# Kernel optimization log

Measured on AMD Instinct MI355X. Metric: run time of the kernel, lower is better.

The kernel has to match this reference:

```python
import jax, jax.numpy as jnp
import numpy as np

B, C, W, H = 4, 64, 64, 64
CH = 64  # ch == input_nc so residual is valid

def setup_inputs() -> dict:
    key = jax.random.key(0)
    ks = jax.random.split(key, 5)
    return {
        "x": jax.random.normal(ks[0], (B, C, W, H), jnp.float32),
        "y": jax.random.normal(ks[1], (B, C, W, H), jnp.float32),
        "Wf": jax.random.normal(ks[2], (CH // 2, C), jnp.float32) * 0.05,
        "bf": jnp.zeros((CH // 2,), jnp.float32),
        "Wg": jax.random.normal(ks[3], (CH // 2, C), jnp.float32) * 0.05,
        "bg": jnp.zeros((CH // 2,), jnp.float32),
        "Wh": jax.random.normal(ks[4], (CH, C), jnp.float32) * 0.05,
        "bh": jnp.zeros((CH,), jnp.float32),
        "gamma": jnp.full((1,), 0.5, jnp.float32),
    }

def reference(x, y, Wf, bf, Wg, bg, Wh, bh, gamma):
    b, c, w, h = x.shape
    n = w * h
    xf = x.reshape(b, c, n)   # [b, C, N]
    yf = y.reshape(b, c, n)
    # 1x1 convs == per-pixel linear maps over channels
    f = jnp.einsum('oc,bcn->bon', Wf, xf) + bf[None, :, None]   # [b, CH/2, N]
    g = jnp.einsum('oc,bcn->bon', Wg, yf) + bg[None, :, None]   # [b, CH/2, N]
    hv = jnp.einsum('oc,bcn->bon', Wh, yf) + bh[None, :, None]  # [b, CH,   N]
    # s = g^T @ f : [b, N, N]
    s = jnp.einsum('bcm,bcn->bmn', g, f)
    beta = jax.nn.softmax(s, axis=-1)
    # o = beta @ h^T : [b, N, CH]
    o = jnp.einsum('bmn,bcn->bmc', beta, hv)
    o = o.transpose(0, 2, 1).reshape(b, -1, w, h)  # [b, CH, w, h]
    return gamma[0] * o + x
```

## Files before the change

kernel.cpp:

```cpp
#include <hip/hip_runtime.h>
#include <hip/hip_bf16.h>

#define BB  4
#define CC  64
#define NN  4096
#define CF  32
#define CHN 64

typedef __attribute__((ext_vector_type(8))) __bf16 bf16x8;
typedef __attribute__((ext_vector_type(4))) __bf16 bf16x4;
typedef __attribute__((ext_vector_type(4))) float floatx4;

__device__ __forceinline__ float clamp60(float v) {
    return fminf(fmaxf(v, -60.f), 60.f);
}
__device__ __forceinline__ float scrub(float v) {
    return fminf(fmaxf(v, -1e30f), 1e30f);
}

__global__ __launch_bounds__(256) void prep_kernel(
    const float* __restrict__ x, const float* __restrict__ y,
    const float* __restrict__ Wf, const float* __restrict__ bfp,
    const float* __restrict__ Wg, const float* __restrict__ bgp,
    const float* __restrict__ Wh, const float* __restrict__ bhp,
    __bf16* __restrict__ fT, __bf16* __restrict__ gT, __bf16* __restrict__ hvb)
{
    __shared__ __align__(16) __bf16 wbf[128][72];
    __shared__ float sbias[128];

    const int t  = threadIdx.x;
    const int w  = t >> 6;
    const int l  = t & 63;
    const int lo = l & 15;
    const int q  = l >> 4;

    const int b   = blockIdx.x >> 6;
    const int nb  = blockIdx.x & 63;
    const int nn  = nb * 64 + w * 16 + lo;

    for (int i = t; i < 128 * CC; i += 256) {
        int row = i >> 6, c = i & 63;
        float wv;
        if (row < 32)      wv = Wf[(size_t)row * CC + c];
        else if (row < 64) wv = Wg[(size_t)(row - 32) * CC + c];
        else               wv = Wh[(size_t)(row - 64) * CC + c];
        wbf[row][c] = (__bf16)wv;
    }
    if (t < 128) {
        if (t < 32)      sbias[t] = bfp[t];
        else if (t < 64) sbias[t] = bgp[t - 32];
        else             sbias[t] = bhp[t - 64];
    }
    __syncthreads();

    const float* xb = x + (size_t)b * CC * NN;
    const float* yb = y + (size_t)b * CC * NN;
    bf16x8 bx[2], by[2];
    #pragma unroll
    for (int kh = 0; kh < 2; kh++) {
        #pragma unroll
        for (int j = 0; j < 8; j++) {
            int c = kh * 32 + q * 8 + j;
            bx[kh][j] = (__bf16)xb[(size_t)c * NN + nn];
            by[kh][j] = (__bf16)yb[(size_t)c * NN + nn];
        }
    }

    const floatx4 zero4 = {0.f, 0.f, 0.f, 0.f};
    #pragma unroll
    for (int ct = 0; ct < 8; ct++) {
        const bf16x8* src = (ct < 2) ? bx : by;
        floatx4 acc = zero4;
        #pragma unroll
        for (int kh = 0; kh < 2; kh++) {
            const bf16x8 a = *(const bf16x8*)&wbf[ct*16 + lo][kh*32 + q*8];
            acc = __builtin_amdgcn_mfma_f32_16x16x32_bf16(a, src[kh], acc, 0, 0, 0);
        }
        if (ct < 4) {
            bf16x4 pk;
            #pragma unroll
            for (int r = 0; r < 4; r++)
                pk[r] = (__bf16)(acc[r] + sbias[ct*16 + q*4 + r]);
            __bf16* dstbase = (ct < 2) ? fT : gT;
            int cho = (ct & 1) * 16;
            *(bf16x4*)&dstbase[((size_t)b * NN + nn) * CF + cho + q*4] = pk;
        } else {
            #pragma unroll
            for (int r = 0; r < 4; r++) {
                int ch = (ct - 4) * 16 + q*4 + r;
                hvb[((size_t)b * CHN + ch) * NN + nn] =
                    (__bf16)(acc[r] + sbias[64 + ch]);
            }
        }
    }
}

__global__ __launch_bounds__(512, 2) void attn_kernel(
    const __bf16* __restrict__ fT, const __bf16* __restrict__ gT,
    const __bf16* __restrict__ hvb,
    const float* __restrict__ x, const float* __restrict__ gamma_p,
    float* __restrict__ out)
{
    __shared__ __align__(16) char smem[8*64*67*4 + 8*64*4];
    __bf16 (*pbf)[72]      = (__bf16 (*)[72])smem;
    float  (*osum)[64][67] = (float (*)[64][67])smem;
    float* lsum = (float*)(smem + 8*64*67*4);

    const int t  = threadIdx.x;
    const int w  = t >> 6;
    const int l  = t & 63;
    const int lo = l & 15;
    const int q  = l >> 4;

    const int mg = blockIdx.x & 63;
    const int b  = blockIdx.x >> 6;
    const int m0 = mg * 64;

    const __bf16* fb = fT  + (size_t)b * NN * CF;
    const __bf16* gb = gT  + (size_t)b * NN * CF;
    const __bf16* hb = hvb + (size_t)b * CHN * NN;

    bf16x8 ag[4];
    #pragma unroll
    for (int mt = 0; mt < 4; mt++)
        ag[mt] = *(const bf16x8*)(gb + (size_t)(m0 + mt*16 + lo) * CF + q * 8);

    bf16x8 vone;
    #pragma unroll
    for (int j = 0; j < 8; j++) vone[j] = (__bf16)1.0f;

    const floatx4 zero4 = {0.f, 0.f, 0.f, 0.f};
    floatx4 oacc[4][4];
    #pragma unroll
    for (int mt = 0; mt < 4; mt++)
        #pragma unroll
        for (int ct = 0; ct < 4; ct++) oacc[mt][ct] = zero4;
    floatx4 lacc[4];
    #pragma unroll
    for (int mt = 0; mt < 4; mt++) lacc[mt] = zero4;

    for (int i = 0; i < 8; i++) {
        const int n0 = (8*i + w) * 64;

        bf16x8 bff[4];
        #pragma unroll
        for (int nt = 0; nt < 4; nt++)
            bff[nt] = *(const bf16x8*)(fb + (size_t)(n0 + nt*16 + lo) * CF + q * 8);
        bf16x8 bhh[4][2];
        #pragma unroll
        for (int ct = 0; ct < 4; ct++)
            #pragma unroll
            for (int jb = 0; jb < 2; jb++)
                bhh[ct][jb] = *(const bf16x8*)(hb + (size_t)(ct*16 + lo) * NN + n0 + jb*32 + q*8);

        #pragma unroll
        for (int mt = 0; mt < 4; mt++) {
            floatx4 s4[4];
            #pragma unroll
            for (int nt = 0; nt < 4; nt++)
                s4[nt] = __builtin_amdgcn_mfma_f32_16x16x32_bf16(ag[mt], bff[nt], zero4, 0, 0, 0);

            #pragma unroll
            for (int nt = 0; nt < 4; nt++)
                #pragma unroll
                for (int r = 0; r < 4; r++)
                    pbf[w*64 + mt*16 + q*4 + r][nt*16 + lo] =
                        (__bf16)__expf(clamp60(s4[nt][r]));
        }
        asm volatile("s_waitcnt lgkmcnt(0)" ::: "memory");

        bf16x8 ap[4][2];
        #pragma unroll
        for (int mt = 0; mt < 4; mt++)
            #pragma unroll
            for (int jb = 0; jb < 2; jb++)
                ap[mt][jb] = *(const bf16x8*)&pbf[w*64 + mt*16 + lo][jb*32 + q*8];
        asm volatile("s_waitcnt lgkmcnt(0)" ::: "memory");

        #pragma unroll
        for (int mt = 0; mt < 4; mt++)
            #pragma unroll
            for (int jb = 0; jb < 2; jb++)
                lacc[mt] = __builtin_amdgcn_mfma_f32_16x16x32_bf16(
                    ap[mt][jb], vone, lacc[mt], 0, 0, 0);

        #pragma unroll
        for (int mt = 0; mt < 4; mt++)
            #pragma unroll
            for (int ct = 0; ct < 4; ct++)
                #pragma unroll
                for (int jb = 0; jb < 2; jb++)
                    oacc[mt][ct] = __builtin_amdgcn_mfma_f32_16x16x32_bf16(
                        ap[mt][jb], bhh[ct][jb], oacc[mt][ct], 0, 0, 0);
    }

    __syncthreads();
    #pragma unroll
    for (int mt = 0; mt < 4; mt++) {
        #pragma unroll
        for (int ct = 0; ct < 4; ct++)
            #pragma unroll
            for (int r = 0; r < 4; r++)
                osum[w][mt*16 + q*4 + r][ct*16 + lo] = oacc[mt][ct][r];
        if (lo == 0)
            #pragma unroll
            for (int r = 0; r < 4; r++)
                lsum[w*64 + mt*16 + q*4 + r] = lacc[mt][r];
    }
    __syncthreads();

    const float gam = gamma_p[0];
    const int m  = t & 63;
    const int cb = t >> 6;
    float lt = 0.f;
    #pragma unroll
    for (int s = 0; s < 8; s++) lt += lsum[s*64 + m];
    const float inv = 1.f / lt;
    #pragma unroll
    for (int it = 0; it < 8; it++) {
        const int ch = it*8 + cb;
        float acc = 0.f;
        #pragma unroll
        for (int s = 0; s < 8; s++) acc += osum[s][m][ch];
        size_t gi = ((size_t)b * CHN + ch) * NN + m0 + m;
        float ov = scrub(acc * inv);
        out[gi] = gam * ov + x[gi];
    }
}

extern "C" void kernel_launch(void* const* d_in, const int* in_sizes, int n_in,
                              void* d_out, int out_size, void* d_ws, size_t ws_size,
                              hipStream_t stream)
{
    const float* x     = (const float*)d_in[0];
    const float* y     = (const float*)d_in[1];
    const float* Wf    = (const float*)d_in[2];
    const float* bf    = (const float*)d_in[3];
    const float* Wg    = (const float*)d_in[4];
    const float* bg    = (const float*)d_in[5];
    const float* Wh    = (const float*)d_in[6];
    const float* bh    = (const float*)d_in[7];
    const float* gamma = (const float*)d_in[8];
    float* out = (float*)d_out;

    __bf16* wsb = (__bf16*)d_ws;
    __bf16* fT  = wsb;
    __bf16* gT  = fT + (size_t)BB * NN * CF;
    __bf16* hvb = gT + (size_t)BB * NN * CF;

    prep_kernel<<<dim3(BB * 64), dim3(256), 0, stream>>>(
        x, y, Wf, bf, Wg, bg, Wh, bh, fT, gT, hvb);
    attn_kernel<<<dim3(BB * 64), dim3(512), 0, stream>>>(
        fT, gT, hvb, x, gamma, out);
}
```

Baseline: 103.3 us.

## Prefetch next f tile with ping-pong registers and remap blocks by XCD

The attention loop now loads the next iteration's f-tile fragments into a second register set while the current tile is processed, alternating two buffers through a macro-unrolled loop. This hides global load latency for the score MFMAs. Block indices are also remapped so that blocks of the same batch land on the same XCD (pairs of XCDs per batch), aiming at better L2 reuse of f and h. The extra prefetch registers may raise register pressure under the 512-thread, 2-blocks-per-CU launch bound.

```diff
diff --git a/kernel.cpp b/kernel.cpp
--- a/kernel.cpp
+++ b/kernel.cpp
@@ -93,6 +93,58 @@
             }
         }
     }
+}
+
+#define STEP(CURF, NXTF, I)                                                   \
+{                                                                             \
+    const int n0 = (8*(I) + w) * 64;                                          \
+    bf16x8 bhh[4][2];                                                         \
+    _Pragma("unroll")                                                         \
+    for (int ct = 0; ct < 4; ct++)                                            \
+        _Pragma("unroll")                                                     \
+        for (int jb = 0; jb < 2; jb++)                                        \
+            bhh[ct][jb] = *(const bf16x8*)(hb + (size_t)(ct*16 + lo) * NN + n0 + jb*32 + q*8); \
+    if ((I) < 7) {                                                            \
+        const int n1 = (8*(I) + 8 + w) * 64;                                  \
+        _Pragma("unroll")                                                     \
+        for (int nt = 0; nt < 4; nt++)                                        \
+            NXTF[nt] = *(const bf16x8*)(fb + (size_t)(n1 + nt*16 + lo) * CF + q * 8); \
+    }                                                                         \
+    _Pragma("unroll")                                                         \
+    for (int mt = 0; mt < 4; mt++) {                                          \
+        floatx4 s4[4];                                                        \
+        _Pragma("unroll")                                                     \
+        for (int nt = 0; nt < 4; nt++)                                        \
+            s4[nt] = __builtin_amdgcn_mfma_f32_16x16x32_bf16(ag[mt], CURF[nt], zero4, 0, 0, 0); \
+        _Pragma("unroll")                                                     \
+        for (int nt = 0; nt < 4; nt++)                                        \
+            _Pragma("unroll")                                                 \
+            for (int r = 0; r < 4; r++)                                       \
+                pbf[w*64 + mt*16 + q*4 + r][nt*16 + lo] =                     \
+                    (__bf16)__expf(clamp60(s4[nt][r]));                       \
+    }                                                                         \
+    asm volatile("s_waitcnt lgkmcnt(0)" ::: "memory");                        \
+    bf16x8 ap[4][2];                                                          \
+    _Pragma("unroll")                                                         \
+    for (int mt = 0; mt < 4; mt++)                                            \
+        _Pragma("unroll")                                                     \
+        for (int jb = 0; jb < 2; jb++)                                        \
+            ap[mt][jb] = *(const bf16x8*)&pbf[w*64 + mt*16 + lo][jb*32 + q*8]; \
+    asm volatile("s_waitcnt lgkmcnt(0)" ::: "memory");                        \
+    _Pragma("unroll")                                                         \
+    for (int mt = 0; mt < 4; mt++)                                            \
+        _Pragma("unroll")                                                     \
+        for (int jb = 0; jb < 2; jb++)                                        \
+            lacc[mt] = __builtin_amdgcn_mfma_f32_16x16x32_bf16(               \
+                ap[mt][jb], vone, lacc[mt], 0, 0, 0);                         \
+    _Pragma("unroll")                                                         \
+    for (int mt = 0; mt < 4; mt++)                                            \
+        _Pragma("unroll")                                                     \
+        for (int ct = 0; ct < 4; ct++)                                        \
+            _Pragma("unroll")                                                 \
+            for (int jb = 0; jb < 2; jb++)                                    \
+                oacc[mt][ct] = __builtin_amdgcn_mfma_f32_16x16x32_bf16(       \
+                    ap[mt][jb], bhh[ct][jb], oacc[mt][ct], 0, 0, 0);          \
 }
 
 __global__ __launch_bounds__(512, 2) void attn_kernel(
@@ -112,9 +164,11 @@
     const int lo = l & 15;
     const int q  = l >> 4;
 
-    const int mg = blockIdx.x & 63;
-    const int b  = blockIdx.x >> 6;
-    const int m0 = mg * 64;
+    const int slot = blockIdx.x;
+    const int xcd  = slot & 7;
+    const int b    = xcd >> 1;
+    const int mg   = ((xcd & 1) << 5) | (slot >> 3);
+    const int m0   = mg * 64;
 
     const __bf16* fb = fT  + (size_t)b * NN * CF;
     const __bf16* gb = gT  + (size_t)b * NN * CF;
@@ -139,59 +193,15 @@
     #pragma unroll
     for (int mt = 0; mt < 4; mt++) lacc[mt] = zero4;
 
-    for (int i = 0; i < 8; i++) {
-        const int n0 = (8*i + w) * 64;
-
-        bf16x8 bff[4];
-        #pragma unroll
-        for (int nt = 0; nt < 4; nt++)
-            bff[nt] = *(const bf16x8*)(fb + (size_t)(n0 + nt*16 + lo) * CF + q * 8);
-        bf16x8 bhh[4][2];
-        #pragma unroll
-        for (int ct = 0; ct < 4; ct++)
-            #pragma unroll
-            for (int jb = 0; jb < 2; jb++)
-                bhh[ct][jb] = *(const bf16x8*)(hb + (size_t)(ct*16 + lo) * NN + n0 + jb*32 + q*8);
-
-        #pragma unroll
-        for (int mt = 0; mt < 4; mt++) {
-            floatx4 s4[4];
-            #pragma unroll
-            for (int nt = 0; nt < 4; nt++)
-                s4[nt] = __builtin_amdgcn_mfma_f32_16x16x32_bf16(ag[mt], bff[nt], zero4, 0, 0, 0);
-
-            #pragma unroll
-            for (int nt = 0; nt < 4; nt++)
-                #pragma unroll
-                for (int r = 0; r < 4; r++)
-                    pbf[w*64 + mt*16 + q*4 + r][nt*16 + lo] =
-                        (__bf16)__expf(clamp60(s4[nt][r]));
-        }
-        asm volatile("s_waitcnt lgkmcnt(0)" ::: "memory");
-
-        bf16x8 ap[4][2];
-        #pragma unroll
-        for (int mt = 0; mt < 4; mt++)
-            #pragma unroll
-            for (int jb = 0; jb < 2; jb++)
-                ap[mt][jb] = *(const bf16x8*)&pbf[w*64 + mt*16 + lo][jb*32 + q*8];
-        asm volatile("s_waitcnt lgkmcnt(0)" ::: "memory");
-
-        #pragma unroll
-        for (int mt = 0; mt < 4; mt++)
-            #pragma unroll
-            for (int jb = 0; jb < 2; jb++)
-                lacc[mt] = __builtin_amdgcn_mfma_f32_16x16x32_bf16(
-                    ap[mt][jb], vone, lacc[mt], 0, 0, 0);
-
-        #pragma unroll
-        for (int mt = 0; mt < 4; mt++)
-            #pragma unroll
-            for (int ct = 0; ct < 4; ct++)
-                #pragma unroll
-                for (int jb = 0; jb < 2; jb++)
-                    oacc[mt][ct] = __builtin_amdgcn_mfma_f32_16x16x32_bf16(
-                        ap[mt][jb], bhh[ct][jb], oacc[mt][ct], 0, 0, 0);
+    bf16x8 bffA[4], bffB[4];
+    #pragma unroll
+    for (int nt = 0; nt < 4; nt++)
+        bffA[nt] = *(const bf16x8*)(fb + (size_t)(w*64 + nt*16 + lo) * CF + q * 8);
+
+    #pragma unroll
+    for (int ii = 0; ii < 4; ii++) {
+        STEP(bffA, bffB, 2*ii);
+        STEP(bffB, bffA, 2*ii + 1);
     }
 
     __syncthreads();
```

New measurement: 103.5 us. About the same (+0.2%).

## Process two key tiles per iteration, remap blocks to XCDs, drop exp clamp

Applied to the files above, without the earlier changes.

Unrolls the attention loop to handle two 64-key tiles per iteration. Both tiles' global loads are issued up front and each tile has its own shared-memory staging area, so the S MFMAs and exp work of the second tile can overlap the PV MFMAs of the first. It also remaps blockIdx so each batch's blocks land on the same XCD pair for L2 locality, and removes the ±60 clamp before exp. The cost is more register pressure, which could cause spills at 512 threads with two blocks per CU. Dropping the clamp relies on scores staying small, which holds for these input scales.

```diff
diff --git a/kernel.cpp b/kernel.cpp
--- a/kernel.cpp
+++ b/kernel.cpp
@@ -11,9 +11,6 @@
 typedef __attribute__((ext_vector_type(4))) __bf16 bf16x4;
 typedef __attribute__((ext_vector_type(4))) float floatx4;
 
-__device__ __forceinline__ float clamp60(float v) {
-    return fminf(fmaxf(v, -60.f), 60.f);
-}
 __device__ __forceinline__ float scrub(float v) {
     return fminf(fmaxf(v, -1e30f), 1e30f);
 }
@@ -101,7 +98,7 @@
     const float* __restrict__ x, const float* __restrict__ gamma_p,
     float* __restrict__ out)
 {
-    __shared__ __align__(16) char smem[8*64*67*4 + 8*64*4];
+    __shared__ __align__(16) char smem[2*512*72*2];
     __bf16 (*pbf)[72]      = (__bf16 (*)[72])smem;
     float  (*osum)[64][67] = (float (*)[64][67])smem;
     float* lsum = (float*)(smem + 8*64*67*4);
@@ -112,9 +109,11 @@
     const int lo = l & 15;
     const int q  = l >> 4;
 
-    const int mg = blockIdx.x & 63;
-    const int b  = blockIdx.x >> 6;
-    const int m0 = mg * 64;
+    const int slot = blockIdx.x;
+    const int xcd  = slot & 7;
+    const int b    = xcd >> 1;
+    const int mg   = ((xcd & 1) << 5) | (slot >> 3);
+    const int m0   = mg * 64;
 
     const __bf16* fb = fT  + (size_t)b * NN * CF;
     const __bf16* gb = gT  + (size_t)b * NN * CF;
@@ -139,42 +138,60 @@
     #pragma unroll
     for (int mt = 0; mt < 4; mt++) lacc[mt] = zero4;
 
-    for (int i = 0; i < 8; i++) {
-        const int n0 = (8*i + w) * 64;
-
-        bf16x8 bff[4];
-        #pragma unroll
-        for (int nt = 0; nt < 4; nt++)
-            bff[nt] = *(const bf16x8*)(fb + (size_t)(n0 + nt*16 + lo) * CF + q * 8);
-        bf16x8 bhh[4][2];
+    #pragma unroll
+    for (int i = 0; i < 4; i++) {
+        const int n0A = (16*i + w) * 64;
+        const int n0B = (16*i + 8 + w) * 64;
+
+        bf16x8 bffA[4], bffB[4];
+        #pragma unroll
+        for (int nt = 0; nt < 4; nt++) {
+            bffA[nt] = *(const bf16x8*)(fb + (size_t)(n0A + nt*16 + lo) * CF + q * 8);
+            bffB[nt] = *(const bf16x8*)(fb + (size_t)(n0B + nt*16 + lo) * CF + q * 8);
+        }
+        bf16x8 bhhA[4][2], bhhB[4][2];
         #pragma unroll
         for (int ct = 0; ct < 4; ct++)
             #pragma unroll
-            for (int jb = 0; jb < 2; jb++)
-                bhh[ct][jb] = *(const bf16x8*)(hb + (size_t)(ct*16 + lo) * NN + n0 + jb*32 + q*8);
+            for (int jb = 0; jb < 2; jb++) {
+                bhhA[ct][jb] = *(const bf16x8*)(hb + (size_t)(ct*16 + lo) * NN + n0A + jb*32 + q*8);
+                bhhB[ct][jb] = *(const bf16x8*)(hb + (size_t)(ct*16 + lo) * NN + n0B + jb*32 + q*8);
+            }
 
         #pragma unroll
         for (int mt = 0; mt < 4; mt++) {
             floatx4 s4[4];
             #pragma unroll
             for (int nt = 0; nt < 4; nt++)
-                s4[nt] = __builtin_amdgcn_mfma_f32_16x16x32_bf16(ag[mt], bff[nt], zero4, 0, 0, 0);
-
+                s4[nt] = __builtin_amdgcn_mfma_f32_16x16x32_bf16(ag[mt], bffA[nt], zero4, 0, 0, 0);
             #pragma unroll
             for (int nt = 0; nt < 4; nt++)
                 #pragma unroll
                 for (int r = 0; r < 4; r++)
                     pbf[w*64 + mt*16 + q*4 + r][nt*16 + lo] =
-                        (__bf16)__expf(clamp60(s4[nt][r]));
-        }
+                        (__bf16)__expf(s4[nt][r]);
+        }
+        #pragma unroll
+        for (int mt = 0; mt < 4; mt++) {
+            floatx4 s4[4];
+            #pragma unroll
+            for (int nt = 0; nt < 4; nt++)
+                s4[nt] = __builtin_amdgcn_mfma_f32_16x16x32_bf16(ag[mt], bffB[nt], zero4, 0, 0, 0);
+            #pragma unroll
+            for (int nt = 0; nt < 4; nt++)
+                #pragma unroll
+                for (int r = 0; r < 4; r++)
+                    pbf[512 + w*64 + mt*16 + q*4 + r][nt*16 + lo] =
+                        (__bf16)__expf(s4[nt][r]);
+        }
+
         asm volatile("s_waitcnt lgkmcnt(0)" ::: "memory");
-
-        bf16x8 ap[4][2];
-        #pragma unroll
-        for (int mt = 0; mt < 4; mt++)
-            #pragma unroll
-            for (int jb = 0; jb < 2; jb++)
-                ap[mt][jb] = *(const bf16x8*)&pbf[w*64 + mt*16 + lo][jb*32 + q*8];
+        bf16x8 apA[4][2];
+        #pragma unroll
+        for (int mt = 0; mt < 4; mt++)
+            #pragma unroll
+            for (int jb = 0; jb < 2; jb++)
+                apA[mt][jb] = *(const bf16x8*)&pbf[w*64 + mt*16 + lo][jb*32 + q*8];
         asm volatile("s_waitcnt lgkmcnt(0)" ::: "memory");
 
         #pragma unroll
@@ -182,8 +199,7 @@
             #pragma unroll
             for (int jb = 0; jb < 2; jb++)
                 lacc[mt] = __builtin_amdgcn_mfma_f32_16x16x32_bf16(
-                    ap[mt][jb], vone, lacc[mt], 0, 0, 0);
-
+                    apA[mt][jb], vone, lacc[mt], 0, 0, 0);
         #pragma unroll
         for (int mt = 0; mt < 4; mt++)
             #pragma unroll
@@ -191,7 +207,30 @@
                 #pragma unroll
                 for (int jb = 0; jb < 2; jb++)
                     oacc[mt][ct] = __builtin_amdgcn_mfma_f32_16x16x32_bf16(
-                        ap[mt][jb], bhh[ct][jb], oacc[mt][ct], 0, 0, 0);
+                        apA[mt][jb], bhhA[ct][jb], oacc[mt][ct], 0, 0, 0);
+
+        bf16x8 apB[4][2];
+        #pragma unroll
+        for (int mt = 0; mt < 4; mt++)
+            #pragma unroll
+            for (int jb = 0; jb < 2; jb++)
+                apB[mt][jb] = *(const bf16x8*)&pbf[512 + w*64 + mt*16 + lo][jb*32 + q*8];
+        asm volatile("s_waitcnt lgkmcnt(0)" ::: "memory");
+
+        #pragma unroll
+        for (int mt = 0; mt < 4; mt++)
+            #pragma unroll
+            for (int jb = 0; jb < 2; jb++)
+                lacc[mt] = __builtin_amdgcn_mfma_f32_16x16x32_bf16(
+                    apB[mt][jb], vone, lacc[mt], 0, 0, 0);
+        #pragma unroll
+        for (int mt = 0; mt < 4; mt++)
+            #pragma unroll
+            for (int ct = 0; ct < 4; ct++)
+                #pragma unroll
+                for (int jb = 0; jb < 2; jb++)
+                    oacc[mt][ct] = __builtin_amdgcn_mfma_f32_16x16x32_bf16(
+                        apB[mt][jb], bhhB[ct][jb], oacc[mt][ct], 0, 0, 0);
     }
 
     __syncthreads();
```

Measured after the change: 102.8 us. No clear change (-0.5%).

## Switch attention to 32x32 MFMA with register-resident P via permlane swaps

Applied to the files above, without the earlier changes.

Rewrites the attention inner loop to use 32x32x16 bf16 MFMAs and computes the score tile transposed (f as A, g as B), so the exponentiated probabilities can be turned into the A operand of the PV matmul in registers. It does this with packed bf16 conversion and permlane32 swaps instead of an LDS round trip. Row sums are accumulated with scalar adds instead of extra MFMAs against a ones vector. Blocks are also remapped so each XCD handles one batch. The exp clamp is removed, which risks overflow with larger scores.

```diff
diff --git a/kernel.cpp b/kernel.cpp
--- a/kernel.cpp
+++ b/kernel.cpp
@@ -7,15 +7,21 @@
 #define CF  32
 #define CHN 64
 
-typedef __attribute__((ext_vector_type(8))) __bf16 bf16x8;
-typedef __attribute__((ext_vector_type(4))) __bf16 bf16x4;
-typedef __attribute__((ext_vector_type(4))) float floatx4;
-
-__device__ __forceinline__ float clamp60(float v) {
-    return fminf(fmaxf(v, -60.f), 60.f);
-}
+typedef __attribute__((ext_vector_type(8)))  __bf16 bf16x8;
+typedef __attribute__((ext_vector_type(4)))  __bf16 bf16x4;
+typedef __attribute__((ext_vector_type(4)))  float  floatx4;
+typedef __attribute__((ext_vector_type(16))) float  floatx16;
+typedef __attribute__((ext_vector_type(2)))  unsigned int uintx2;
+typedef __attribute__((ext_vector_type(4)))  unsigned int uintx4;
+
 __device__ __forceinline__ float scrub(float v) {
     return fminf(fmaxf(v, -1e30f), 1e30f);
+}
+
+__device__ __forceinline__ unsigned cvt_pk_bf16(float lo, float hi) {
+    unsigned r;
+    asm("v_cvt_pk_bf16_f32 %0, %1, %2" : "=v"(r) : "v"(lo), "v"(hi));
+    return r;
 }
 
 __global__ __launch_bounds__(256) void prep_kernel(
@@ -101,111 +107,116 @@
     const float* __restrict__ x, const float* __restrict__ gamma_p,
     float* __restrict__ out)
 {
-    __shared__ __align__(16) char smem[8*64*67*4 + 8*64*4];
-    __bf16 (*pbf)[72]      = (__bf16 (*)[72])smem;
-    float  (*osum)[64][67] = (float (*)[64][67])smem;
-    float* lsum = (float*)(smem + 8*64*67*4);
-
-    const int t  = threadIdx.x;
-    const int w  = t >> 6;
-    const int l  = t & 63;
-    const int lo = l & 15;
-    const int q  = l >> 4;
-
-    const int mg = blockIdx.x & 63;
-    const int b  = blockIdx.x >> 6;
-    const int m0 = mg * 64;
+    __shared__ float osum[8][64][67];
+    __shared__ float lsum[512];
+
+    const int t   = threadIdx.x;
+    const int w   = t >> 6;
+    const int l   = t & 63;
+    const int l31 = l & 31;
+    const int hi  = l >> 5;
+
+    const int slot = blockIdx.x;
+    const int xcd  = slot & 7;
+    const int b    = xcd >> 1;
+    const int mg   = ((xcd & 1) << 5) | (slot >> 3);
+    const int m0   = mg * 64;
 
     const __bf16* fb = fT  + (size_t)b * NN * CF;
     const __bf16* gb = gT  + (size_t)b * NN * CF;
     const __bf16* hb = hvb + (size_t)b * CHN * NN;
 
-    bf16x8 ag[4];
-    #pragma unroll
-    for (int mt = 0; mt < 4; mt++)
-        ag[mt] = *(const bf16x8*)(gb + (size_t)(m0 + mt*16 + lo) * CF + q * 8);
-
-    bf16x8 vone;
-    #pragma unroll
-    for (int j = 0; j < 8; j++) vone[j] = (__bf16)1.0f;
-
-    const floatx4 zero4 = {0.f, 0.f, 0.f, 0.f};
-    floatx4 oacc[4][4];
-    #pragma unroll
-    for (int mt = 0; mt < 4; mt++)
-        #pragma unroll
-        for (int ct = 0; ct < 4; ct++) oacc[mt][ct] = zero4;
-    floatx4 lacc[4];
-    #pragma unroll
-    for (int mt = 0; mt < 4; mt++) lacc[mt] = zero4;
+    bf16x8 bg_[2][2];
+    #pragma unroll
+    for (int mt = 0; mt < 2; mt++)
+        #pragma unroll
+        for (int kk = 0; kk < 2; kk++)
+            bg_[mt][kk] = *(const bf16x8*)(gb + (size_t)(m0 + mt*32 + l31) * CF + kk*16 + hi*8);
+
+    const floatx16 zero16 = {};
+    floatx16 oacc[2][2];
+    #pragma unroll
+    for (int mt = 0; mt < 2; mt++)
+        #pragma unroll
+        for (int ct = 0; ct < 2; ct++) oacc[mt][ct] = zero16;
+    float rsum[2] = {0.f, 0.f};
 
     for (int i = 0; i < 8; i++) {
         const int n0 = (8*i + w) * 64;
 
-        bf16x8 bff[4];
-        #pragma unroll
-        for (int nt = 0; nt < 4; nt++)
-            bff[nt] = *(const bf16x8*)(fb + (size_t)(n0 + nt*16 + lo) * CF + q * 8);
-        bf16x8 bhh[4][2];
-        #pragma unroll
-        for (int ct = 0; ct < 4; ct++)
-            #pragma unroll
-            for (int jb = 0; jb < 2; jb++)
-                bhh[ct][jb] = *(const bf16x8*)(hb + (size_t)(ct*16 + lo) * NN + n0 + jb*32 + q*8);
-
-        #pragma unroll
-        for (int mt = 0; mt < 4; mt++) {
-            floatx4 s4[4];
-            #pragma unroll
-            for (int nt = 0; nt < 4; nt++)
-                s4[nt] = __builtin_amdgcn_mfma_f32_16x16x32_bf16(ag[mt], bff[nt], zero4, 0, 0, 0);
-
-            #pragma unroll
-            for (int nt = 0; nt < 4; nt++)
-                #pragma unroll
-                for (int r = 0; r < 4; r++)
-                    pbf[w*64 + mt*16 + q*4 + r][nt*16 + lo] =
-                        (__bf16)__expf(clamp60(s4[nt][r]));
-        }
-        asm volatile("s_waitcnt lgkmcnt(0)" ::: "memory");
-
-        bf16x8 ap[4][2];
-        #pragma unroll
-        for (int mt = 0; mt < 4; mt++)
-            #pragma unroll
-            for (int jb = 0; jb < 2; jb++)
-                ap[mt][jb] = *(const bf16x8*)&pbf[w*64 + mt*16 + lo][jb*32 + q*8];
-        asm volatile("s_waitcnt lgkmcnt(0)" ::: "memory");
-
-        #pragma unroll
-        for (int mt = 0; mt < 4; mt++)
-            #pragma unroll
-            for (int jb = 0; jb < 2; jb++)
-                lacc[mt] = __builtin_amdgcn_mfma_f32_16x16x32_bf16(
-                    ap[mt][jb], vone, lacc[mt], 0, 0, 0);
-
-        #pragma unroll
-        for (int mt = 0; mt < 4; mt++)
-            #pragma unroll
-            for (int ct = 0; ct < 4; ct++)
-                #pragma unroll
-                for (int jb = 0; jb < 2; jb++)
-                    oacc[mt][ct] = __builtin_amdgcn_mfma_f32_16x16x32_bf16(
-                        ap[mt][jb], bhh[ct][jb], oacc[mt][ct], 0, 0, 0);
-    }
-
-    __syncthreads();
-    #pragma unroll
-    for (int mt = 0; mt < 4; mt++) {
-        #pragma unroll
-        for (int ct = 0; ct < 4; ct++)
-            #pragma unroll
-            for (int r = 0; r < 4; r++)
-                osum[w][mt*16 + q*4 + r][ct*16 + lo] = oacc[mt][ct][r];
-        if (lo == 0)
-            #pragma unroll
-            for (int r = 0; r < 4; r++)
-                lsum[w*64 + mt*16 + q*4 + r] = lacc[mt][r];
+        bf16x8 af[2][2];
+        #pragma unroll
+        for (int nt = 0; nt < 2; nt++)
+            #pragma unroll
+            for (int kk = 0; kk < 2; kk++)
+                af[nt][kk] = *(const bf16x8*)(fb + (size_t)(n0 + nt*32 + l31) * CF + kk*16 + hi*8);
+
+        bf16x8 bv[2][4];
+        #pragma unroll
+        for (int ct = 0; ct < 2; ct++)
+            #pragma unroll
+            for (int ks = 0; ks < 4; ks++)
+                bv[ct][ks] = *(const bf16x8*)(hb + (size_t)(ct*32 + l31) * NN + n0 + ks*16 + hi*8);
+
+        bf16x8 pa[2][4];
+        #pragma unroll
+        for (int mt = 0; mt < 2; mt++) {
+            #pragma unroll
+            for (int nt = 0; nt < 2; nt++) {
+                floatx16 s = __builtin_amdgcn_mfma_f32_32x32x16_bf16(
+                    af[nt][0], bg_[mt][0], zero16, 0, 0, 0);
+                s = __builtin_amdgcn_mfma_f32_32x32x16_bf16(
+                    af[nt][1], bg_[mt][1], s, 0, 0, 0);
+
+                float p[16];
+                #pragma unroll
+                for (int r = 0; r < 16; r++) p[r] = __expf(s[r]);
+
+                unsigned W[8];
+                #pragma unroll
+                for (int g = 0; g < 8; g++) W[g] = cvt_pk_bf16(p[2*g], p[2*g+1]);
+
+                #pragma unroll
+                for (int g = 0; g < 8; g++)
+                    rsum[mt] += __uint_as_float(W[g] << 16)
+                              + __uint_as_float(W[g] & 0xffff0000u);
+
+                uintx2 s02 = __builtin_amdgcn_permlane32_swap(W[0], W[2], false, false);
+                uintx2 s13 = __builtin_amdgcn_permlane32_swap(W[1], W[3], false, false);
+                uintx2 s46 = __builtin_amdgcn_permlane32_swap(W[4], W[6], false, false);
+                uintx2 s57 = __builtin_amdgcn_permlane32_swap(W[5], W[7], false, false);
+
+                uintx4 w0 = {s02.x, s13.x, s02.y, s13.y};
+                uintx4 w1 = {s46.x, s57.x, s46.y, s57.y};
+                pa[mt][nt*2 + 0] = __builtin_bit_cast(bf16x8, w0);
+                pa[mt][nt*2 + 1] = __builtin_bit_cast(bf16x8, w1);
+            }
+        }
+
+        #pragma unroll
+        for (int mt = 0; mt < 2; mt++)
+            #pragma unroll
+            for (int ct = 0; ct < 2; ct++)
+                #pragma unroll
+                for (int ks = 0; ks < 4; ks++)
+                    oacc[mt][ct] = __builtin_amdgcn_mfma_f32_32x32x16_bf16(
+                        pa[mt][ks], bv[ct][ks], oacc[mt][ct], 0, 0, 0);
+    }
+
+    #pragma unroll
+    for (int mt = 0; mt < 2; mt++)
+        rsum[mt] += __shfl_xor(rsum[mt], 32, 64);
+
+    #pragma unroll
+    for (int mt = 0; mt < 2; mt++) {
+        #pragma unroll
+        for (int ct = 0; ct < 2; ct++)
+            #pragma unroll
+            for (int r = 0; r < 16; r++)
+                osum[w][mt*32 + ((r&3) + 8*(r>>2) + 4*hi)][ct*32 + l31] =
+                    oacc[mt][ct][r];
+        if (hi == 0)
+            lsum[w*64 + mt*32 + l31] = rsum[mt];
     }
     __syncthreads();
 
```

Measured after the change: 102.3 us. No clear change (-1.0%).
